# Kernel optimization log

Hardware: AMD Instinct MI355X
Metric: run time of the kernel (lower is better)

The kernel has to match this reference:

```python
import jax, jax.numpy as jnp
import numpy as np

BATCH, SEQ_LEN, D_MODEL, STATE_DIM = 8, 4096, 512, 64
LN_EPS = 1e-5


def _hippo_log_neg_eigs(state_dim):
    A = np.zeros((state_dim, state_dim))
    for i in range(state_dim):
        for j in range(state_dim):
            if i > j:
                A[i, j] = -((2 * i + 1) ** 0.5) * ((2 * j + 1) ** 0.5)
            elif i == j:
                A[i, j] = -(i + 1)
    ev = np.sort(np.linalg.eigvals(A).real)[:state_dim]
    return np.log(-ev + 1e-06).astype(np.float32)


def setup_inputs() -> dict:
    key = jax.random.key(0)
    ks = jax.random.split(key, 8)
    d, s = D_MODEL, STATE_DIM
    return {
        "x": jax.random.normal(ks[0], (BATCH, SEQ_LEN, d), dtype=jnp.float32),
        "log_A": jnp.asarray(_hippo_log_neg_eigs(s)),
        "B": jax.random.normal(ks[1], (d, s), dtype=jnp.float32) * 0.01,
        "C": jax.random.normal(ks[2], (s, d), dtype=jnp.float32) * 0.01,
        "D": jnp.zeros((d,), dtype=jnp.float32),
        "log_dt": jnp.zeros((), dtype=jnp.float32),
        "gamma": jnp.ones((d,), dtype=jnp.float32),
        "beta": jnp.zeros((d,), dtype=jnp.float32),
        "W1": jax.random.normal(ks[3], (d, 2 * d), dtype=jnp.float32) * (1.0 / np.sqrt(d)),
        "b1": jnp.zeros((2 * d,), dtype=jnp.float32),
        "W2": jax.random.normal(ks[4], (2 * d, d), dtype=jnp.float32) * (1.0 / np.sqrt(2 * d)),
        "b2": jnp.zeros((d,), dtype=jnp.float32),
    }


def _layernorm(x, gamma, beta):
    mu = jnp.mean(x, axis=-1, keepdims=True)
    var = jnp.mean(jnp.square(x - mu), axis=-1, keepdims=True)
    return (x - mu) * jax.lax.rsqrt(var + LN_EPS) * gamma + beta


def reference(x, log_A, B, C, D, log_dt, gamma, beta, W1, b1, W2, b2):
    residual = x
    xn = _layernorm(x, gamma, beta)  # [B, L, D]

    dt = jnp.exp(log_dt)
    A_bar = jnp.exp(-jnp.exp(log_A) * dt)  # [S]

    # Precompute input projections for all timesteps, then scan the diagonal recurrence.
    xB = jnp.einsum("bld,ds->lbs", xn, B)  # [L, B, S]
    h0 = jnp.zeros((xn.shape[0], A_bar.shape[0]), dtype=xn.dtype)

    def step(h, xb_t):
        h = A_bar * h + xb_t
        return h, h

    _, hs = jax.lax.scan(step, h0, xB)  # hs: [L, B, S]

    y = jnp.einsum("lbs,sd->bld", hs, C) + xn * D  # [B, L, D]
    y = y + residual

    yn = _layernorm(y, gamma, beta)
    mlp = jax.nn.gelu(yn @ W1 + b1, approximate=False) @ W2 + b2
    return y + mlp
```

## Files before the change

kernel.cpp:

```cpp
#include <hip/hip_runtime.h>
#include <math.h>

#define BATCH 8
#define SEQL 4096
#define DMODEL 512
#define SDIM 64
#define MROWS (BATCH * SEQL)
#define LN_EPS 1e-5f

typedef __attribute__((ext_vector_type(8))) short bf16x8;
typedef __attribute__((ext_vector_type(4))) float f32x4;
typedef __attribute__((ext_vector_type(4))) int i32x4;

__device__ __forceinline__ float wave_sum(float v) {
#pragma unroll
  for (int off = 32; off > 0; off >>= 1) v += __shfl_xor(v, off, 64);
  return v;
}

__device__ __forceinline__ unsigned short f2bf(float f) {
  unsigned int u = __float_as_uint(f);
  u += 0x7fffu + ((u >> 16) & 1u);
  return (unsigned short)(u >> 16);
}

__device__ __forceinline__ float gelu_fast(float v) {
  float s = v * 0.70710678118654752f;
  float ax = fabsf(s);
  float t = 1.0f / (1.0f + 0.3275911f * ax);
  float p = ((((1.061405429f * t - 1.453152027f) * t + 1.421413741f) * t - 0.284496736f) * t +
             0.254829592f) *
            t;
  float er = 1.0f - p * __expf(-ax * ax);
  er = copysignf(er, s);
  return 0.5f * v * (1.0f + er);
}

__device__ __forceinline__ void gl2lds16(const void* g, void* l) {
  __builtin_amdgcn_global_load_lds((const __attribute__((address_space(1))) void*)g,
                                   (__attribute__((address_space(3))) void*)l, 16, 0, 0);
}

__device__ __forceinline__ unsigned lds_addr(const void* p) {
  return (unsigned)(uintptr_t)(__attribute__((address_space(3))) const void*)p;
}

__device__ __forceinline__ bf16x8 ldsr128(unsigned addr) {
  i32x4 r;
  asm volatile("ds_read_b128 %0, %1" : "=v"(r) : "v"(addr));
  union {
    i32x4 i;
    bf16x8 h;
  } u;
  u.i = r;
  return u.h;
}

__global__ void ln_stats_kernel(const float* __restrict__ x, float* __restrict__ mu,
                                float* __restrict__ rstd, unsigned short* __restrict__ xbf) {
  int row = blockIdx.x * 4 + (threadIdx.x >> 6);
  int lane = threadIdx.x & 63;
  const float4* xp = (const float4*)(x + (size_t)row * DMODEL);
  float4 a = xp[lane * 2];
  float4 b = xp[lane * 2 + 1];
  float s = a.x + a.y + a.z + a.w + b.x + b.y + b.z + b.w;
  float q = a.x * a.x + a.y * a.y + a.z * a.z + a.w * a.w + b.x * b.x + b.y * b.y +
            b.z * b.z + b.w * b.w;
  s = wave_sum(s);
  q = wave_sum(q);
  uint4 pk;
  pk.x = (unsigned)f2bf(a.x) | ((unsigned)f2bf(a.y) << 16);
  pk.y = (unsigned)f2bf(a.z) | ((unsigned)f2bf(a.w) << 16);
  pk.z = (unsigned)f2bf(b.x) | ((unsigned)f2bf(b.y) << 16);
  pk.w = (unsigned)f2bf(b.z) | ((unsigned)f2bf(b.w) << 16);
  ((uint4*)(xbf + (size_t)row * DMODEL))[lane] = pk;
  if (lane == 0) {
    float m = s * (1.0f / DMODEL);
    float var = q * (1.0f / DMODEL) - m * m;
    mu[row] = m;
    rstd[row] = rsqrtf(var + LN_EPS);
  }
}

__device__ __forceinline__ void transpose_body(const float* __restrict__ W,
                                               unsigned short* __restrict__ Wt, int K, int N,
                                               int bx, int by,
                                               unsigned short (*tile)[65]) {
  int k0 = by * 64, n0 = bx * 64;
  int tx = threadIdx.x & 15, ty = threadIdx.x >> 4;
#pragma unroll
  for (int p = 0; p < 4; ++p) {
    int k = p * 16 + ty;
    float4 v = *(const float4*)&W[(size_t)(k0 + k) * N + n0 + tx * 4];
    tile[tx * 4 + 0][k] = f2bf(v.x);
    tile[tx * 4 + 1][k] = f2bf(v.y);
    tile[tx * 4 + 2][k] = f2bf(v.z);
    tile[tx * 4 + 3][k] = f2bf(v.w);
  }
  __syncthreads();
#pragma unroll
  for (int p = 0; p < 4; ++p) {
    int n = p * 16 + ty;
    ushort4 o;
    o.x = tile[n][tx * 4 + 0];
    o.y = tile[n][tx * 4 + 1];
    o.z = tile[n][tx * 4 + 2];
    o.w = tile[n][tx * 4 + 3];
    *(ushort4*)&Wt[(size_t)(n0 + n) * K + k0 + tx * 4] = o;
  }
}

__global__ __launch_bounds__(256) void prep_all_kernel(
    const float* __restrict__ W1, const float* __restrict__ W2, const float* __restrict__ Cm,
    const float* __restrict__ Bm, const float* __restrict__ gamma,
    const float* __restrict__ beta, unsigned short* __restrict__ w1t,
    unsigned short* __restrict__ w2t, unsigned short* __restrict__ ctb,
    unsigned short* __restrict__ Bgt, float* __restrict__ gB, float* __restrict__ bB) {
  __shared__ unsigned short tile[64][65];
  int b = blockIdx.x;
  if (b < 128) {
    transpose_body(W1, w1t, 512, 1024, b & 15, b >> 4, tile);
  } else if (b < 256) {
    transpose_body(W2, w2t, 1024, 512, (b - 128) & 7, (b - 128) >> 3, tile);
  } else if (b < 264) {
    transpose_body(Cm, ctb, 64, 512, b - 256, 0, tile);
  } else {
    int s = (b - 264) * 4 + (threadIdx.x >> 6);
    int l = threadIdx.x & 63;
    float gs = 0.0f, bs = 0.0f;
    unsigned short tmp[8];
#pragma unroll
    for (int u = 0; u < 8; ++u) {
      int d = l * 8 + u;
      float bv = Bm[(size_t)d * SDIM + s];
      float gv = gamma[d], ev = beta[d];
      gs += gv * bv;
      bs += ev * bv;
      tmp[u] = f2bf(gv * bv);
    }
    *(ushort4*)&Bgt[(size_t)s * DMODEL + l * 8] = make_ushort4(tmp[0], tmp[1], tmp[2], tmp[3]);
    *(ushort4*)&Bgt[(size_t)s * DMODEL + l * 8 + 4] =
        make_ushort4(tmp[4], tmp[5], tmp[6], tmp[7]);
    gs = wave_sum(gs);
    bs = wave_sum(bs);
    if (l == 0) {
      gB[s] = gs;
      bB[s] = bs;
    }
  }
}

__global__ __launch_bounds__(256) void xb_mfma_kernel(
    const unsigned short* __restrict__ xbf, const unsigned short* __restrict__ Bgt,
    const float* __restrict__ mu, const float* __restrict__ rstd, const float* __restrict__ gB,
    const float* __restrict__ bB, float* __restrict__ xB) {
  __shared__ unsigned short As[128 * 32];
  __shared__ unsigned short Bs[64 * 32];
  const int t = threadIdx.x;
  const int wave = t >> 6, lane = t & 63;
  const int m0 = blockIdx.x * 128;
  const int wm = wave * 32;
  const int row = t >> 2, seg = t & 3;
  const int fr = lane & 15, fq = lane >> 4;
  f32x4 acc[2][4] = {};
  for (int k0 = 0; k0 < DMODEL; k0 += 32) {
    __syncthreads();
    gl2lds16(xbf + (size_t)(m0 + row) * DMODEL + k0 + seg * 8, As + (size_t)(wave * 16) * 32);
    gl2lds16(xbf + (size_t)(m0 + 64 + row) * DMODEL + k0 + seg * 8,
             As + (size_t)(64 + wave * 16) * 32);
    gl2lds16(Bgt + (size_t)row * DMODEL + k0 + seg * 8, Bs + (size_t)(wave * 16) * 32);
    __syncthreads();
#pragma unroll
    for (int i = 0; i < 2; ++i) {
      bf16x8 a = *(const bf16x8*)&As[(wm + i * 16 + fr) * 32 + fq * 8];
#pragma unroll
      for (int j = 0; j < 4; ++j) {
        bf16x8 b = *(const bf16x8*)&Bs[(j * 16 + fr) * 32 + fq * 8];
        acc[i][j] = __builtin_amdgcn_mfma_f32_16x16x32_bf16(a, b, acc[i][j], 0, 0, 0);
      }
    }
  }
#pragma unroll
  for (int i = 0; i < 2; ++i)
#pragma unroll
    for (int r = 0; r < 4; ++r) {
      const int m = m0 + wm + i * 16 + fq * 4 + r;
      const float rr = rstd[m], negmurr = -mu[m] * rstd[m];
#pragma unroll
      for (int j = 0; j < 4; ++j) {
        const int s = j * 16 + fr;
        xB[(size_t)m * SDIM + s] = rr * acc[i][j][r] + negmurr * gB[s] + bB[s];
      }
    }
}

__global__ void scan_ends_kernel(const float* __restrict__ xB, const float* __restrict__ logA,
                                 const float* __restrict__ logdt, float* __restrict__ ends) {
  int t = blockIdx.x * 256 + threadIdx.x;
  int s = t & 63;
  int c = (t >> 6) & 63;
  int b = t >> 12;
  float a = expf(-expf(logA[s]) * expf(logdt[0]));
  const float* p = xB + ((size_t)(b * SEQL + c * 64)) * SDIM + s;
  float e = 0.0f;
#pragma unroll
  for (int i = 0; i < 64; ++i) e = a * e + p[(size_t)i * SDIM];
  ends[(b * 64 + c) * 64 + s] = e;
}

__global__ void scan_fix_kernel(const float* __restrict__ logA, const float* __restrict__ logdt,
                                const float* __restrict__ ends, const float* __restrict__ xB,
                                unsigned short* __restrict__ hsb) {
  int t = blockIdx.x * 256 + threadIdx.x;
  int s = t & 63;
  int c = (t >> 6) & 63;
  int b = t >> 12;
  float a = expf(-expf(logA[s]) * expf(logdt[0]));
  float a64 = a;
#pragma unroll
  for (int i = 0; i < 6; ++i) a64 *= a64;
  float h = 0.0f;
  for (int cp = 0; cp < c; ++cp) h = a64 * h + ends[(b * 64 + cp) * 64 + s];
  const float* p = xB + ((size_t)(b * SEQL + c * 64)) * SDIM + s;
  unsigned short* q = hsb + ((size_t)(b * SEQL + c * 64)) * SDIM + s;
#pragma unroll
  for (int i = 0; i < 64; ++i) {
    h = a * h + p[(size_t)i * SDIM];
    q[(size_t)i * SDIM] = f2bf(h);
  }
}

__global__ __launch_bounds__(256) void y_gemm_mfma_kernel(
    const unsigned short* __restrict__ hsb, const unsigned short* __restrict__ ctb,
    const float* __restrict__ x, const float* __restrict__ mu1,
    const float* __restrict__ rstd1, const float* __restrict__ gamma,
    const float* __restrict__ beta, const float* __restrict__ Dv, float* __restrict__ out) {
  __shared__ unsigned short As[2 * 128 * 32];
  __shared__ unsigned short Bs[2 * 128 * 32];
  const int t = threadIdx.x;
  const int w = t >> 6, lane = t & 63;
  const int m0 = blockIdx.y * 128, n0 = blockIdx.x * 128;
  const int wm = (w >> 1) * 64, wn = (w & 1) * 64;
  const int fr = lane & 15, fq = lane >> 4;
  const int srow = t >> 2, sseg = t & 3;
#pragma unroll
  for (int h = 0; h < 2; ++h)
#pragma unroll
    for (int c = 0; c < 2; ++c) {
      gl2lds16(hsb + (size_t)(m0 + c * 64 + srow) * SDIM + h * 32 + sseg * 8,
               As + ((size_t)h * 128 + c * 64 + w * 16) * 32);
      gl2lds16(ctb + (size_t)(n0 + c * 64 + srow) * SDIM + h * 32 + sseg * 8,
               Bs + ((size_t)h * 128 + c * 64 + w * 16) * 32);
    }
  __syncthreads();
  f32x4 acc[4][4] = {};
#pragma unroll
  for (int h = 0; h < 2; ++h) {
    bf16x8 a[4], b[4];
#pragma unroll
    for (int i = 0; i < 4; ++i)
      a[i] = *(const bf16x8*)&As[((size_t)h * 128 + wm + i * 16 + fr) * 32 + fq * 8];
#pragma unroll
    for (int j = 0; j < 4; ++j)
      b[j] = *(const bf16x8*)&Bs[((size_t)h * 128 + wn + j * 16 + fr) * 32 + fq * 8];
#pragma unroll
    for (int i = 0; i < 4; ++i)
#pragma unroll
      for (int j = 0; j < 4; ++j)
        acc[i][j] = __builtin_amdgcn_mfma_f32_16x16x32_bf16(a[i], b[j], acc[i][j], 0, 0, 0);
  }
  float mm[4][4], rr[4][4];
#pragma unroll
  for (int i = 0; i < 4; ++i)
#pragma unroll
    for (int r = 0; r < 4; ++r) {
      int m = m0 + wm + i * 16 + fq * 4 + r;
      mm[i][r] = mu1[m];
      rr[i][r] = rstd1[m];
    }
#pragma unroll
  for (int j = 0; j < 4; ++j) {
    const int n = n0 + wn + j * 16 + fr;
    const float ga = gamma[n], be = beta[n], dd = Dv[n];
#pragma unroll
    for (int i = 0; i < 4; ++i) {
      float xv[4];
#pragma unroll
      for (int r = 0; r < 4; ++r)
        xv[r] = x[(size_t)(m0 + wm + i * 16 + fq * 4 + r) * DMODEL + n];
#pragma unroll
      for (int r = 0; r < 4; ++r) {
        float yv = acc[i][j][r] + ((xv[r] - mm[i][r]) * rr[i][r] * ga + be) * dd + xv[r];
        out[(size_t)(m0 + wm + i * 16 + fq * 4 + r) * DMODEL + n] = yv;
      }
    }
  }
}

__global__ void ln_apply_kernel(const float* __restrict__ y, const float* __restrict__ gamma,
                                const float* __restrict__ beta,
                                unsigned short* __restrict__ yn) {
  int row = blockIdx.x * 4 + (threadIdx.x >> 6);
  int lane = threadIdx.x & 63;
  const float4* yp = (const float4*)(y + (size_t)row * DMODEL);
  float4 a = yp[lane * 2];
  float4 b = yp[lane * 2 + 1];
  float s = a.x + a.y + a.z + a.w + b.x + b.y + b.z + b.w;
  float q = a.x * a.x + a.y * a.y + a.z * a.z + a.w * a.w + b.x * b.x + b.y * b.y +
            b.z * b.z + b.w * b.w;
  s = wave_sum(s);
  q = wave_sum(q);
  float m = s * (1.0f / DMODEL);
  float var = q * (1.0f / DMODEL) - m * m;
  float rs = rsqrtf(var + LN_EPS);
  const float4* gp = (const float4*)gamma;
  const float4* bp = (const float4*)beta;
  float4 g0 = gp[lane * 2], g1 = gp[lane * 2 + 1];
  float4 e0 = bp[lane * 2], e1 = bp[lane * 2 + 1];
  float o0x = (a.x - m) * rs * g0.x + e0.x, o0y = (a.y - m) * rs * g0.y + e0.y;
  float o0z = (a.z - m) * rs * g0.z + e0.z, o0w = (a.w - m) * rs * g0.w + e0.w;
  float o1x = (b.x - m) * rs * g1.x + e1.x, o1y = (b.y - m) * rs * g1.y + e1.y;
  float o1z = (b.z - m) * rs * g1.z + e1.z, o1w = (b.w - m) * rs * g1.w + e1.w;
  uint4 pk;
  pk.x = (unsigned)f2bf(o0x) | ((unsigned)f2bf(o0y) << 16);
  pk.y = (unsigned)f2bf(o0z) | ((unsigned)f2bf(o0w) << 16);
  pk.z = (unsigned)f2bf(o1x) | ((unsigned)f2bf(o1y) << 16);
  pk.w = (unsigned)f2bf(o1z) | ((unsigned)f2bf(o1w) << 16);
  ((uint4*)(yn + (size_t)row * DMODEL))[lane] = pk;
}

template <int K, int NALL, int EPI>
__global__ __launch_bounds__(512, 2) void gemm256_kernel(
    const unsigned short* __restrict__ Am, const unsigned short* __restrict__ Bm,
    const float* __restrict__ bias, unsigned short* __restrict__ gout,
    float* __restrict__ out) {
  __shared__ alignas(16) unsigned short As[2][256 * 64];
  __shared__ alignas(16) unsigned short Bs[2][256 * 64];
  const int t = threadIdx.x;
  const int wid = t >> 6, lane = t & 63;
  const int nwg = gridDim.x * gridDim.y;
  const int orig = blockIdx.y * gridDim.x + blockIdx.x;
  const int swz = (orig & 7) * (nwg >> 3) + (orig >> 3);
  const int m0 = (swz / gridDim.x) * 256, n0 = (swz % gridDim.x) * 256;
  const int wm = (wid >> 2) * 128, wn = (wid & 3) * 64;
  const int fr = lane & 15, fq = lane >> 4;
  constexpr int NT = K / 64;
  const int srow = t >> 3;
  const int ksw = ((t & 7) ^ ((t >> 3) & 7)) << 3;

  auto stageA = [&](int bb, int h, int kt) {
    const unsigned short* s0 = Am + (size_t)(m0 + h * 128 + srow) * K + kt * 64 + ksw;
    gl2lds16(s0, &As[bb][(h * 128 + wid * 8) * 64]);
    gl2lds16(s0 + (size_t)64 * K, &As[bb][(h * 128 + 64 + wid * 8) * 64]);
  };
  auto stageB = [&](int bb, int h, int kt) {
    const unsigned short* s0 = Bm + (size_t)(n0 + h * 128 + srow) * K + kt * 64 + ksw;
    gl2lds16(s0, &Bs[bb][(h * 128 + wid * 8) * 64]);
    gl2lds16(s0 + (size_t)64 * K, &Bs[bb][(h * 128 + 64 + wid * 8) * 64]);
  };

  const unsigned aA0 = lds_addr(&As[0][0]) + (unsigned)((wm + fr) * 128 + (fq ^ (fr & 7)) * 16);
  const unsigned aA1 =
      lds_addr(&As[0][0]) + (unsigned)((wm + fr) * 128 + ((4 + fq) ^ (fr & 7)) * 16);
  const unsigned aB0 = lds_addr(&Bs[0][0]) + (unsigned)((wn + fr) * 128 + (fq ^ (fr & 7)) * 16);
  const unsigned aB1 =
      lds_addr(&Bs[0][0]) + (unsigned)((wn + fr) * 128 + ((4 + fq) ^ (fr & 7)) * 16);

  stageA(0, 0, 0);
  stageA(0, 1, 0);
  stageB(0, 0, 0);
  stageB(0, 1, 0);
  stageB(1, 0, 1);
  stageB(1, 1, 1);
  asm volatile("s_waitcnt vmcnt(4)" ::: "memory");
  __builtin_amdgcn_s_barrier();

  f32x4 acc[8][4] = {};
  for (int c = 0; c < NT; ++c) {
    const int b = c & 1;
    const unsigned bo = (unsigned)(b * 32768);
    bf16x8 bfr[2][4];
#pragma unroll
    for (int q = 0; q < 4; ++q) {
      bf16x8 a2[2][2];
      a2[0][0] = ldsr128(aA0 + bo + (2 * q) * 2048);
      a2[0][1] = ldsr128(aA1 + bo + (2 * q) * 2048);
      a2[1][0] = ldsr128(aA0 + bo + (2 * q + 1) * 2048);
      a2[1][1] = ldsr128(aA1 + bo + (2 * q + 1) * 2048);
      if (q == 0) {
#pragma unroll
        for (int j = 0; j < 4; ++j) {
          bfr[0][j] = ldsr128(aB0 + bo + j * 2048);
          bfr[1][j] = ldsr128(aB1 + bo + j * 2048);
        }
        if (c + 1 < NT) stageA(b ^ 1, 0, c + 1);
      } else if (q == 1) {
        if (c + 1 < NT) stageA(b ^ 1, 1, c + 1);
      } else if (q == 2) {
        if (c + 2 < NT) stageB(b, 0, c + 2);
      } else {
        if (c + 2 < NT) stageB(b, 1, c + 2);
      }
      __builtin_amdgcn_s_barrier();
      asm volatile("s_waitcnt lgkmcnt(0)" ::: "memory");
      __builtin_amdgcn_sched_barrier(0);
      __builtin_amdgcn_s_setprio(1);
#pragma unroll
      for (int ii = 0; ii < 2; ++ii)
#pragma unroll
        for (int s = 0; s < 2; ++s)
#pragma unroll
          for (int j = 0; j < 4; ++j)
            acc[2 * q + ii][j] = __builtin_amdgcn_mfma_f32_16x16x32_bf16(
                a2[ii][s], bfr[s][j], acc[2 * q + ii][j], 0, 0, 0);
      __builtin_amdgcn_s_setprio(0);
      if (q < 3) {
        __builtin_amdgcn_s_barrier();
      } else if (c < NT - 1) {
        if (c < NT - 2)
          asm volatile("s_waitcnt vmcnt(4)" ::: "memory");
        else
          asm volatile("s_waitcnt vmcnt(0)" ::: "memory");
        __builtin_amdgcn_s_barrier();
      }
    }
  }

#pragma unroll
  for (int i = 0; i < 8; ++i)
#pragma unroll
    for (int j = 0; j < 4; ++j) {
      const int cg = n0 + wn + j * 16 + fr;
      const float bb = bias[cg];
#pragma unroll
      for (int r = 0; r < 4; ++r) {
        const int rg = m0 + wm + i * 16 + fq * 4 + r;
        if (EPI == 0) {
          gout[(size_t)rg * NALL + cg] = f2bf(gelu_fast(acc[i][j][r] + bb));
        } else {
          const size_t off = (size_t)rg * NALL + cg;
          out[off] = out[off] + acc[i][j][r] + bb;
        }
      }
    }
}

extern "C" void kernel_launch(void* const* d_in, const int* in_sizes, int n_in, void* d_out,
                              int out_size, void* d_ws, size_t ws_size, hipStream_t stream) {
  const float* x = (const float*)d_in[0];
  const float* logA = (const float*)d_in[1];
  const float* Bm = (const float*)d_in[2];
  const float* Cm = (const float*)d_in[3];
  const float* Dv = (const float*)d_in[4];
  const float* logdt = (const float*)d_in[5];
  const float* gamma = (const float*)d_in[6];
  const float* beta = (const float*)d_in[7];
  const float* W1 = (const float*)d_in[8];
  const float* b1 = (const float*)d_in[9];
  const float* W2 = (const float*)d_in[10];
  const float* b2 = (const float*)d_in[11];
  float* out = (float*)d_out;

  char* ws = (char*)d_ws;
  float* mu1 = (float*)(ws + 0);
  float* rstd1 = (float*)(ws + 131072);
  float* ends = (float*)(ws + 262144);
  float* gB = (float*)(ws + 524288);
  float* bB = (float*)(ws + 524800);
  unsigned short* Bgt = (unsigned short*)(ws + 525312);
  unsigned short* ctb = (unsigned short*)(ws + 590848);
  unsigned short* w1t = (unsigned short*)(ws + 656384);
  unsigned short* w2t = (unsigned short*)(ws + 1704960);
  unsigned short* g = (unsigned short*)(ws + 2753536);
  unsigned short* xbf = (unsigned short*)(ws + 2753536);
  float* xB = (float*)(ws + 69862400);
  unsigned short* hsb = (unsigned short*)(ws + 78251008);
  unsigned short* yn = (unsigned short*)(ws + 82445312);

  prep_all_kernel<<<280, 256, 0, stream>>>(W1, W2, Cm, Bm, gamma, beta, w1t, w2t, ctb, Bgt, gB,
                                           bB);
  ln_stats_kernel<<<MROWS / 4, 256, 0, stream>>>(x, mu1, rstd1, xbf);
  xb_mfma_kernel<<<MROWS / 128, 256, 0, stream>>>(xbf, Bgt, mu1, rstd1, gB, bB, xB);
  scan_ends_kernel<<<128, 256, 0, stream>>>(xB, logA, logdt, ends);
  scan_fix_kernel<<<128, 256, 0, stream>>>(logA, logdt, ends, xB, hsb);
  y_gemm_mfma_kernel<<<dim3(DMODEL / 128, MROWS / 128), 256, 0, stream>>>(
      hsb, ctb, x, mu1, rstd1, gamma, beta, Dv, out);
  ln_apply_kernel<<<MROWS / 4, 256, 0, stream>>>(out, gamma, beta, yn);
  gemm256_kernel<512, 1024, 0><<<dim3(1024 / 256, MROWS / 256), 512, 0, stream>>>(
      yn, w1t, b1, g, nullptr);
  gemm256_kernel<1024, 512, 1><<<dim3(512 / 256, MROWS / 256), 512, 0, stream>>>(
      g, w2t, b2, nullptr, out);
}
```

Before: 318.4 us.

## Fuse y GEMM with second LayerNorm, repipeline MLP GEMM, shrink scan blocks

Merges the C-projection GEMM with the residual epilogue and the second LayerNorm. Each block now computes full 128x512 rows, reduces row statistics through LDS atomics and writes the bf16 normalized activations directly, so the separate ln_apply pass and its re-read of y are gone. The 256-tile MLP GEMM main loop is restructured into a two-half register double-buffered schedule that prefetches one stage ahead instead of two, with fewer barriers per K tile. The scan kernels switch to 128-thread blocks with twice as many blocks, which spreads the latency-bound recurrence over more CUs. The fused kernel has large register and LDS use (acc[4][8] per thread, 80KB shared memory), which may limit occupancy, and the shallower prefetch may expose load latency in the large GEMMs.

```diff
diff --git a/kernel.cpp b/kernel.cpp
--- a/kernel.cpp
+++ b/kernel.cpp
@@ -196,7 +196,7 @@
 
 __global__ void scan_ends_kernel(const float* __restrict__ xB, const float* __restrict__ logA,
                                  const float* __restrict__ logdt, float* __restrict__ ends) {
-  int t = blockIdx.x * 256 + threadIdx.x;
+  int t = blockIdx.x * 128 + threadIdx.x;
   int s = t & 63;
   int c = (t >> 6) & 63;
   int b = t >> 12;
@@ -211,7 +211,7 @@
 __global__ void scan_fix_kernel(const float* __restrict__ logA, const float* __restrict__ logdt,
                                 const float* __restrict__ ends, const float* __restrict__ xB,
                                 unsigned short* __restrict__ hsb) {
-  int t = blockIdx.x * 256 + threadIdx.x;
+  int t = blockIdx.x * 128 + threadIdx.x;
   int s = t & 63;
   int c = (t >> 6) & 63;
   int b = t >> 12;
@@ -230,103 +230,116 @@
   }
 }
 
-__global__ __launch_bounds__(256) void y_gemm_mfma_kernel(
+__global__ __launch_bounds__(512, 2) void y_ln_fused_kernel(
     const unsigned short* __restrict__ hsb, const unsigned short* __restrict__ ctb,
     const float* __restrict__ x, const float* __restrict__ mu1,
     const float* __restrict__ rstd1, const float* __restrict__ gamma,
-    const float* __restrict__ beta, const float* __restrict__ Dv, float* __restrict__ out) {
-  __shared__ unsigned short As[2 * 128 * 32];
-  __shared__ unsigned short Bs[2 * 128 * 32];
+    const float* __restrict__ beta, const float* __restrict__ Dv, float* __restrict__ out,
+    unsigned short* __restrict__ yn) {
+  __shared__ alignas(16) unsigned short As[128 * 64];
+  __shared__ alignas(16) unsigned short Bs[512 * 64];
+  __shared__ float rsum[128], rsq[128];
   const int t = threadIdx.x;
-  const int w = t >> 6, lane = t & 63;
-  const int m0 = blockIdx.y * 128, n0 = blockIdx.x * 128;
-  const int wm = (w >> 1) * 64, wn = (w & 1) * 64;
+  const int wid = t >> 6, lane = t & 63;
+  const int m0 = blockIdx.x * 128;
+  const int wm = (wid >> 2) * 64;
+  const int wn = (wid & 3) * 128;
   const int fr = lane & 15, fq = lane >> 4;
-  const int srow = t >> 2, sseg = t & 3;
-#pragma unroll
-  for (int h = 0; h < 2; ++h)
-#pragma unroll
-    for (int c = 0; c < 2; ++c) {
-      gl2lds16(hsb + (size_t)(m0 + c * 64 + srow) * SDIM + h * 32 + sseg * 8,
-               As + ((size_t)h * 128 + c * 64 + w * 16) * 32);
-      gl2lds16(ctb + (size_t)(n0 + c * 64 + srow) * SDIM + h * 32 + sseg * 8,
-               Bs + ((size_t)h * 128 + c * 64 + w * 16) * 32);
-    }
+  const int srow = t >> 3;
+  const int ksw = ((t & 7) ^ ((t >> 3) & 7)) << 3;
+  gl2lds16(hsb + (size_t)(m0 + srow) * 64 + ksw, &As[(wid * 8) * 64]);
+  gl2lds16(hsb + (size_t)(m0 + 64 + srow) * 64 + ksw, &As[(64 + wid * 8) * 64]);
+#pragma unroll
+  for (int h = 0; h < 8; ++h)
+    gl2lds16(ctb + (size_t)(h * 64 + srow) * 64 + ksw, &Bs[(h * 64 + wid * 8) * 64]);
+  if (t < 128) {
+    rsum[t] = 0.0f;
+    rsq[t] = 0.0f;
+  }
+  asm volatile("s_waitcnt vmcnt(0)" ::: "memory");
+  __builtin_amdgcn_s_barrier();
+
+  f32x4 acc[4][8] = {};
+#pragma unroll
+  for (int s = 0; s < 2; ++s) {
+    bf16x8 af[4], bf[8];
+#pragma unroll
+    for (int i = 0; i < 4; ++i)
+      af[i] = *(const bf16x8*)&As[(wm + i * 16 + fr) * 64 + ((s * 4 + fq) ^ (fr & 7)) * 8];
+#pragma unroll
+    for (int j = 0; j < 8; ++j)
+      bf[j] = *(const bf16x8*)&Bs[(wn + j * 16 + fr) * 64 + ((s * 4 + fq) ^ (fr & 7)) * 8];
+#pragma unroll
+    for (int i = 0; i < 4; ++i)
+#pragma unroll
+      for (int j = 0; j < 8; ++j)
+        acc[i][j] = __builtin_amdgcn_mfma_f32_16x16x32_bf16(af[i], bf[j], acc[i][j], 0, 0, 0);
+  }
+
+  float ga[8], be[8], dd[8];
+#pragma unroll
+  for (int j = 0; j < 8; ++j) {
+    const int cg = wn + j * 16 + fr;
+    ga[j] = gamma[cg];
+    be[j] = beta[cg];
+    dd[j] = Dv[cg];
+  }
+  float ps[4][4], pq[4][4];
+#pragma unroll
+  for (int i = 0; i < 4; ++i)
+#pragma unroll
+    for (int r = 0; r < 4; ++r) {
+      const int m = m0 + wm + i * 16 + fq * 4 + r;
+      const float mu = mu1[m], rs = rstd1[m];
+      float s1 = 0.0f, s2 = 0.0f;
+#pragma unroll
+      for (int j = 0; j < 8; ++j) {
+        const int cg = wn + j * 16 + fr;
+        const float xv = x[(size_t)m * DMODEL + cg];
+        float yv = acc[i][j][r] + ((xv - mu) * rs * ga[j] + be[j]) * dd[j] + xv;
+        out[(size_t)m * DMODEL + cg] = yv;
+        acc[i][j][r] = yv;
+        s1 += yv;
+        s2 += yv * yv;
+      }
+      ps[i][r] = s1;
+      pq[i][r] = s2;
+    }
+#pragma unroll
+  for (int i = 0; i < 4; ++i)
+#pragma unroll
+    for (int r = 0; r < 4; ++r) {
+#pragma unroll
+      for (int off = 1; off < 16; off <<= 1) {
+        ps[i][r] += __shfl_xor(ps[i][r], off, 64);
+        pq[i][r] += __shfl_xor(pq[i][r], off, 64);
+      }
+    }
+  if (fr == 0) {
+#pragma unroll
+    for (int i = 0; i < 4; ++i)
+#pragma unroll
+      for (int r = 0; r < 4; ++r) {
+        atomicAdd(&rsum[wm + i * 16 + fq * 4 + r], ps[i][r]);
+        atomicAdd(&rsq[wm + i * 16 + fq * 4 + r], pq[i][r]);
+      }
+  }
   __syncthreads();
-  f32x4 acc[4][4] = {};
-#pragma unroll
-  for (int h = 0; h < 2; ++h) {
-    bf16x8 a[4], b[4];
-#pragma unroll
-    for (int i = 0; i < 4; ++i)
-      a[i] = *(const bf16x8*)&As[((size_t)h * 128 + wm + i * 16 + fr) * 32 + fq * 8];
-#pragma unroll
-    for (int j = 0; j < 4; ++j)
-      b[j] = *(const bf16x8*)&Bs[((size_t)h * 128 + wn + j * 16 + fr) * 32 + fq * 8];
-#pragma unroll
-    for (int i = 0; i < 4; ++i)
-#pragma unroll
-      for (int j = 0; j < 4; ++j)
-        acc[i][j] = __builtin_amdgcn_mfma_f32_16x16x32_bf16(a[i], b[j], acc[i][j], 0, 0, 0);
-  }
-  float mm[4][4], rr[4][4];
 #pragma unroll
   for (int i = 0; i < 4; ++i)
 #pragma unroll
     for (int r = 0; r < 4; ++r) {
-      int m = m0 + wm + i * 16 + fq * 4 + r;
-      mm[i][r] = mu1[m];
-      rr[i][r] = rstd1[m];
-    }
-#pragma unroll
-  for (int j = 0; j < 4; ++j) {
-    const int n = n0 + wn + j * 16 + fr;
-    const float ga = gamma[n], be = beta[n], dd = Dv[n];
-#pragma unroll
-    for (int i = 0; i < 4; ++i) {
-      float xv[4];
-#pragma unroll
-      for (int r = 0; r < 4; ++r)
-        xv[r] = x[(size_t)(m0 + wm + i * 16 + fq * 4 + r) * DMODEL + n];
-#pragma unroll
-      for (int r = 0; r < 4; ++r) {
-        float yv = acc[i][j][r] + ((xv[r] - mm[i][r]) * rr[i][r] * ga + be) * dd + xv[r];
-        out[(size_t)(m0 + wm + i * 16 + fq * 4 + r) * DMODEL + n] = yv;
-      }
-    }
-  }
-}
-
-__global__ void ln_apply_kernel(const float* __restrict__ y, const float* __restrict__ gamma,
-                                const float* __restrict__ beta,
-                                unsigned short* __restrict__ yn) {
-  int row = blockIdx.x * 4 + (threadIdx.x >> 6);
-  int lane = threadIdx.x & 63;
-  const float4* yp = (const float4*)(y + (size_t)row * DMODEL);
-  float4 a = yp[lane * 2];
-  float4 b = yp[lane * 2 + 1];
-  float s = a.x + a.y + a.z + a.w + b.x + b.y + b.z + b.w;
-  float q = a.x * a.x + a.y * a.y + a.z * a.z + a.w * a.w + b.x * b.x + b.y * b.y +
-            b.z * b.z + b.w * b.w;
-  s = wave_sum(s);
-  q = wave_sum(q);
-  float m = s * (1.0f / DMODEL);
-  float var = q * (1.0f / DMODEL) - m * m;
-  float rs = rsqrtf(var + LN_EPS);
-  const float4* gp = (const float4*)gamma;
-  const float4* bp = (const float4*)beta;
-  float4 g0 = gp[lane * 2], g1 = gp[lane * 2 + 1];
-  float4 e0 = bp[lane * 2], e1 = bp[lane * 2 + 1];
-  float o0x = (a.x - m) * rs * g0.x + e0.x, o0y = (a.y - m) * rs * g0.y + e0.y;
-  float o0z = (a.z - m) * rs * g0.z + e0.z, o0w = (a.w - m) * rs * g0.w + e0.w;
-  float o1x = (b.x - m) * rs * g1.x + e1.x, o1y = (b.y - m) * rs * g1.y + e1.y;
-  float o1z = (b.z - m) * rs * g1.z + e1.z, o1w = (b.w - m) * rs * g1.w + e1.w;
-  uint4 pk;
-  pk.x = (unsigned)f2bf(o0x) | ((unsigned)f2bf(o0y) << 16);
-  pk.y = (unsigned)f2bf(o0z) | ((unsigned)f2bf(o0w) << 16);
-  pk.z = (unsigned)f2bf(o1x) | ((unsigned)f2bf(o1y) << 16);
-  pk.w = (unsigned)f2bf(o1z) | ((unsigned)f2bf(o1w) << 16);
-  ((uint4*)(yn + (size_t)row * DMODEL))[lane] = pk;
+      const int rl = wm + i * 16 + fq * 4 + r;
+      const int m = m0 + rl;
+      const float mu2 = rsum[rl] * (1.0f / DMODEL);
+      const float var = rsq[rl] * (1.0f / DMODEL) - mu2 * mu2;
+      const float rs2 = rsqrtf(var + LN_EPS);
+#pragma unroll
+      for (int j = 0; j < 8; ++j) {
+        const int cg = wn + j * 16 + fr;
+        yn[(size_t)m * DMODEL + cg] = f2bf((acc[i][j][r] - mu2) * rs2 * ga[j] + be[j]);
+      }
+    }
 }
 
 template <int K, int NALL, int EPI>
@@ -370,60 +383,60 @@
   stageA(0, 1, 0);
   stageB(0, 0, 0);
   stageB(0, 1, 0);
-  stageB(1, 0, 1);
-  stageB(1, 1, 1);
-  asm volatile("s_waitcnt vmcnt(4)" ::: "memory");
+  asm volatile("s_waitcnt vmcnt(0)" ::: "memory");
   __builtin_amdgcn_s_barrier();
+
+  bf16x8 a0[8], b0[4], a1[8], b1[4];
+#pragma unroll
+  for (int i = 0; i < 8; ++i) a0[i] = ldsr128(aA0 + i * 2048);
+#pragma unroll
+  for (int j = 0; j < 4; ++j) b0[j] = ldsr128(aB0 + j * 2048);
 
   f32x4 acc[8][4] = {};
   for (int c = 0; c < NT; ++c) {
-    const int b = c & 1;
-    const unsigned bo = (unsigned)(b * 32768);
-    bf16x8 bfr[2][4];
-#pragma unroll
-    for (int q = 0; q < 4; ++q) {
-      bf16x8 a2[2][2];
-      a2[0][0] = ldsr128(aA0 + bo + (2 * q) * 2048);
-      a2[0][1] = ldsr128(aA1 + bo + (2 * q) * 2048);
-      a2[1][0] = ldsr128(aA0 + bo + (2 * q + 1) * 2048);
-      a2[1][1] = ldsr128(aA1 + bo + (2 * q + 1) * 2048);
-      if (q == 0) {
-#pragma unroll
-        for (int j = 0; j < 4; ++j) {
-          bfr[0][j] = ldsr128(aB0 + bo + j * 2048);
-          bfr[1][j] = ldsr128(aB1 + bo + j * 2048);
-        }
-        if (c + 1 < NT) stageA(b ^ 1, 0, c + 1);
-      } else if (q == 1) {
-        if (c + 1 < NT) stageA(b ^ 1, 1, c + 1);
-      } else if (q == 2) {
-        if (c + 2 < NT) stageB(b, 0, c + 2);
-      } else {
-        if (c + 2 < NT) stageB(b, 1, c + 2);
-      }
+    const unsigned bo = (unsigned)((c & 1) << 15);
+    const unsigned bn = bo ^ 32768u;
+#pragma unroll
+    for (int i = 0; i < 8; ++i) a1[i] = ldsr128(aA1 + bo + i * 2048);
+#pragma unroll
+    for (int j = 0; j < 4; ++j) b1[j] = ldsr128(aB1 + bo + j * 2048);
+    if (c + 1 < NT) {
+      const int nb = (c & 1) ^ 1;
+      stageA(nb, 0, c + 1);
+      stageA(nb, 1, c + 1);
+      stageB(nb, 0, c + 1);
+      stageB(nb, 1, c + 1);
+    }
+    asm volatile("s_waitcnt lgkmcnt(12)" ::: "memory");
+    __builtin_amdgcn_sched_barrier(0);
+    __builtin_amdgcn_s_setprio(1);
+#pragma unroll
+    for (int i = 0; i < 8; ++i)
+#pragma unroll
+      for (int j = 0; j < 4; ++j)
+        acc[i][j] = __builtin_amdgcn_mfma_f32_16x16x32_bf16(a0[i], b0[j], acc[i][j], 0, 0, 0);
+    __builtin_amdgcn_s_setprio(0);
+    __builtin_amdgcn_sched_barrier(0);
+    if (c + 1 < NT) {
+      asm volatile("s_waitcnt vmcnt(0)" ::: "memory");
       __builtin_amdgcn_s_barrier();
+#pragma unroll
+      for (int i = 0; i < 8; ++i) a0[i] = ldsr128(aA0 + bn + i * 2048);
+#pragma unroll
+      for (int j = 0; j < 4; ++j) b0[j] = ldsr128(aB0 + bn + j * 2048);
+      asm volatile("s_waitcnt lgkmcnt(12)" ::: "memory");
+    } else {
       asm volatile("s_waitcnt lgkmcnt(0)" ::: "memory");
-      __builtin_amdgcn_sched_barrier(0);
-      __builtin_amdgcn_s_setprio(1);
-#pragma unroll
-      for (int ii = 0; ii < 2; ++ii)
-#pragma unroll
-        for (int s = 0; s < 2; ++s)
-#pragma unroll
-          for (int j = 0; j < 4; ++j)
-            acc[2 * q + ii][j] = __builtin_amdgcn_mfma_f32_16x16x32_bf16(
-                a2[ii][s], bfr[s][j], acc[2 * q + ii][j], 0, 0, 0);
-      __builtin_amdgcn_s_setprio(0);
-      if (q < 3) {
-        __builtin_amdgcn_s_barrier();
-      } else if (c < NT - 1) {
-        if (c < NT - 2)
-          asm volatile("s_waitcnt vmcnt(4)" ::: "memory");
-        else
-          asm volatile("s_waitcnt vmcnt(0)" ::: "memory");
-        __builtin_amdgcn_s_barrier();
-      }
-    }
+    }
+    __builtin_amdgcn_sched_barrier(0);
+    __builtin_amdgcn_s_setprio(1);
+#pragma unroll
+    for (int i = 0; i < 8; ++i)
+#pragma unroll
+      for (int j = 0; j < 4; ++j)
+        acc[i][j] = __builtin_amdgcn_mfma_f32_16x16x32_bf16(a1[i], b1[j], acc[i][j], 0, 0, 0);
+    __builtin_amdgcn_s_setprio(0);
+    if (c + 1 < NT) __builtin_amdgcn_s_barrier();
   }
 
 #pragma unroll
@@ -481,11 +494,10 @@
                                            bB);
   ln_stats_kernel<<<MROWS / 4, 256, 0, stream>>>(x, mu1, rstd1, xbf);
   xb_mfma_kernel<<<MROWS / 128, 256, 0, stream>>>(xbf, Bgt, mu1, rstd1, gB, bB, xB);
-  scan_ends_kernel<<<128, 256, 0, stream>>>(xB, logA, logdt, ends);
-  scan_fix_kernel<<<128, 256, 0, stream>>>(logA, logdt, ends, xB, hsb);
-  y_gemm_mfma_kernel<<<dim3(DMODEL / 128, MROWS / 128), 256, 0, stream>>>(
-      hsb, ctb, x, mu1, rstd1, gamma, beta, Dv, out);
-  ln_apply_kernel<<<MROWS / 4, 256, 0, stream>>>(out, gamma, beta, yn);
+  scan_ends_kernel<<<256, 128, 0, stream>>>(xB, logA, logdt, ends);
+  scan_fix_kernel<<<256, 128, 0, stream>>>(logA, logdt, ends, xB, hsb);
+  y_ln_fused_kernel<<<MROWS / 128, 512, 0, stream>>>(hsb, ctb, x, mu1, rstd1, gamma, beta, Dv,
+                                                     out, yn);
   gemm256_kernel<512, 1024, 0><<<dim3(1024 / 256, MROWS / 256), 512, 0, stream>>>(
       yn, w1t, b1, g, nullptr);
   gemm256_kernel<1024, 512, 1><<<dim3(512 / 256, MROWS / 256), 512, 0, stream>>>(
```

Measured after the change: 321.2 us. Within noise of the previous version (+0.9%).
